# Optimization experiments

Hardware: AMD Instinct MI355X
Metric: run time of the kernel (lower is better)

## Reference

```python
import jax, jax.numpy as jnp
import numpy as np

B, C, H, W = 8, 512, 64, 32
SE_MID = C // 16
BN_EPS = 1e-5


def conv1x1(x, w, b):
    # x: [B,Cin,H,W], w: [Cout,Cin], b: [Cout]
    return jnp.einsum('bchw,oc->bohw', x, w) + b[None, :, None, None]


def setup_inputs() -> dict:
    key = jax.random.key(0)
    ks = jax.random.split(key, 17)
    s = 0.05
    return {
        'x': jax.random.normal(ks[0], (B, C, H, W), jnp.float32),
        'g_w': jax.random.normal(ks[1], (1, C), jnp.float32) * s,
        'g_b': jax.random.normal(ks[2], (1,), jnp.float32) * s,
        'theta_w': jax.random.normal(ks[3], (1, C), jnp.float32) * s,
        'theta_b': jax.random.normal(ks[4], (1,), jnp.float32) * s,
        'phi_w': jax.random.normal(ks[5], (1, C), jnp.float32) * s,
        'phi_b': jax.random.normal(ks[6], (1,), jnp.float32) * s,
        'W_w': jax.random.normal(ks[7], (C, 1), jnp.float32) * s,
        'W_b': jax.random.normal(ks[8], (C,), jnp.float32) * s,
        'bn_gamma': jax.random.normal(ks[9], (C,), jnp.float32) * s + 1.0,
        'bn_beta': jax.random.normal(ks[10], (C,), jnp.float32) * s,
        'bn_mean': jax.random.normal(ks[11], (C,), jnp.float32) * s,
        'bn_var': jax.random.uniform(ks[12], (C,), jnp.float32, 0.5, 1.5),
        'se1_w': jax.random.normal(ks[13], (SE_MID, C), jnp.float32) * s,
        'se1_b': jnp.zeros((SE_MID,), jnp.float32),
        'se2_w': jax.random.normal(ks[14], (C, SE_MID), jnp.float32) * s,
        'se2_b': jnp.zeros((C,), jnp.float32),
    }


def reference(x, g_w, g_b, theta_w, theta_b, phi_w, phi_b, W_w, W_b,
              bn_gamma, bn_beta, bn_mean, bn_var, se1_w, se1_b, se2_w, se2_b):
    b, c, h, w = x.shape
    N = h * w
    # SE channel gate from global average pool: [B,C,1,1]
    x_avg = jnp.mean(x, axis=(2, 3), keepdims=True)
    se_mid = jax.nn.relu(conv1x1(x_avg, se1_w, se1_b))
    W_cw = jax.nn.sigmoid(conv1x1(se_mid, se2_w, se2_b))  # [B,C,1,1]

    # inter_channels == 1: each projection is a length-N vector per sample
    g_x = conv1x1(x, g_w, g_b).reshape(b, N)          # [B,N]
    theta_x = conv1x1(x, theta_w, theta_b).reshape(b, N)  # [B,N]
    phi_x = conv1x1(x, phi_w, phi_b).reshape(b, N)        # [B,N]

    # f[b,i,j] = theta[b,i] * phi[b,j]; row softmax over j; y = f_div_C @ g
    f = theta_x[:, :, None] * phi_x[:, None, :]       # [B,N,N]
    f_div_C = jax.nn.softmax(f, axis=-1)
    y = jnp.einsum('bij,bj->bi', f_div_C, g_x)        # [B,N]
    y = y.reshape(b, 1, h, w)

    # W: 1x1 conv (1 -> C) + BatchNorm2d (inference form with running stats)
    W_y = conv1x1(y, W_w, W_b)                        # [B,C,H,W]
    inv = bn_gamma / jnp.sqrt(bn_var + BN_EPS)
    W_y = (W_y - bn_mean[None, :, None, None]) * inv[None, :, None, None] \
          + bn_beta[None, :, None, None]

    return W_cw * W_y + x
```

## Files before the change

kernel.cpp:

```cpp
#include <hip/hip_runtime.h>

#define BB 8
#define CC 512
#define NN 2048
#define SEM 32
#define BN_EPS 1e-5f

#define NCC 16
#define NCHUNK (CC / NCC)
#define PIX 1024

__global__ __launch_bounds__(256) void k1(const float* __restrict__ x,
    const float* __restrict__ gw, const float* __restrict__ tw, const float* __restrict__ pw,
    float* __restrict__ pp,
    float* __restrict__ avgp)
{
    int tid = threadIdx.x;
    int wave = tid >> 6, lane = tid & 63;
    int blk = blockIdx.x;
    int ic = blk & 1;
    int cc = (blk >> 1) & (NCHUNK - 1);
    int b  = blk >> 6;
    int c0 = cc * NCC;

    const float4* xp = reinterpret_cast<const float4*>(x)
                     + ((size_t)(b * CC + c0) * (NN / 4)) + ic * (PIX / 4);

    float4 ag = {0,0,0,0}, at_ = {0,0,0,0}, ap = {0,0,0,0};

    #pragma unroll 4
    for (int c = 0; c < NCC; ++c) {
        float4 v = xp[(size_t)c * (NN / 4) + tid];
        float wgc = gw[c0 + c], wtc = tw[c0 + c], wpc = pw[c0 + c];
        ag.x = fmaf(wgc, v.x, ag.x); ag.y = fmaf(wgc, v.y, ag.y);
        ag.z = fmaf(wgc, v.z, ag.z); ag.w = fmaf(wgc, v.w, ag.w);
        at_.x = fmaf(wtc, v.x, at_.x); at_.y = fmaf(wtc, v.y, at_.y);
        at_.z = fmaf(wtc, v.z, at_.z); at_.w = fmaf(wtc, v.w, at_.w);
        ap.x = fmaf(wpc, v.x, ap.x); ap.y = fmaf(wpc, v.y, ap.y);
        ap.z = fmaf(wpc, v.z, ap.z); ap.w = fmaf(wpc, v.w, ap.w);
        float s = (v.x + v.y) + (v.z + v.w);
        for (int o = 32; o > 0; o >>= 1) s += __shfl_down(s, o);
        if (lane == 0)
            avgp[(size_t)(b * CC + c0 + c) * 8 + ic * 4 + wave] = s;
    }

    size_t base = (((size_t)b * 2 + ic) * NCHUNK + cc) * PIX + tid * 4;
    const size_t karr = (size_t)BB * 2 * NCHUNK * PIX;
    *reinterpret_cast<float4*>(pp + 0 * karr + base) = ag;
    *reinterpret_cast<float4*>(pp + 1 * karr + base) = at_;
    *reinterpret_cast<float4*>(pp + 2 * karr + base) = ap;
}

__global__ __launch_bounds__(256) void k2(
    const float* __restrict__ pp, const float* __restrict__ avgp,
    const float* __restrict__ gb, const float* __restrict__ tb, const float* __restrict__ pb,
    const float* __restrict__ se1w, const float* __restrict__ se1b,
    const float* __restrict__ se2w, const float* __restrict__ se2b,
    const float* __restrict__ Ww, const float* __restrict__ Wb,
    const float* __restrict__ gamma, const float* __restrict__ beta,
    const float* __restrict__ mean, const float* __restrict__ var,
    float* __restrict__ gx, float* __restrict__ tx, float* __restrict__ px,
    float* __restrict__ Ac, float* __restrict__ Dc)
{
    int tid = threadIdx.x;
    if (blockIdx.x < 64) {
        int q  = blockIdx.x & 3;
        int ic = (blockIdx.x >> 2) & 1;
        int b  = blockIdx.x >> 3;
        int p  = q * 256 + tid;
        size_t base = (((size_t)b * 2 + ic) * NCHUNK) * PIX + p;
        const size_t karr = (size_t)BB * 2 * NCHUNK * PIX;
        float g = 0.f, t = 0.f, ph = 0.f;
        #pragma unroll 8
        for (int cc = 0; cc < NCHUNK; ++cc) {
            g  += pp[0 * karr + base + cc * PIX];
            t  += pp[1 * karr + base + cc * PIX];
            ph += pp[2 * karr + base + cc * PIX];
        }
        int o = b * NN + ic * PIX + p;
        gx[o] = g + gb[0];
        tx[o] = t + tb[0];
        px[o] = ph + pb[0];
        return;
    }

    int b = blockIdx.x - 64;
    __shared__ float sA[CC];
    __shared__ float sP[SEM][8];
    __shared__ float sM[SEM];
    for (int c = tid; c < CC; c += 256) {
        const float* ap = avgp + (size_t)(b * CC + c) * 8;
        float s = 0.f;
        #pragma unroll
        for (int k = 0; k < 8; ++k) s += ap[k];
        sA[c] = s * (1.0f / NN);
    }
    __syncthreads();
    {
        int m = tid >> 3, sub = tid & 7;
        const float* w1 = se1w + m * CC + sub * 64;
        const float* a1 = sA + sub * 64;
        float s = 0.f;
        #pragma unroll
        for (int k = 0; k < 64; ++k) s = fmaf(a1[k], w1[k], s);
        sP[m][sub] = s;
    }
    __syncthreads();
    if (tid < SEM) {
        float t = 0.f;
        #pragma unroll
        for (int k = 0; k < 8; ++k) t += sP[tid][k];
        sM[tid] = fmaxf(t + se1b[tid], 0.f);
    }
    __syncthreads();
    for (int c = tid; c < CC; c += 256) {
        float s2 = 0.f;
        #pragma unroll
        for (int m = 0; m < SEM; ++m) s2 = fmaf(sM[m], se2w[c * SEM + m], s2);
        s2 += se2b[c];
        float wcw = 1.f / (1.f + __expf(-s2));
        float inv = gamma[c] * rsqrtf(var[c] + BN_EPS);
        Ac[b * CC + c] = wcw * Ww[c] * inv;
        Dc[b * CC + c] = wcw * ((Wb[c] - mean[c]) * inv + beta[c]);
    }
}

__global__ __launch_bounds__(256) void k3(
    const float* __restrict__ gx, const float* __restrict__ tx,
    const float* __restrict__ px, float* __restrict__ y)
{
    __shared__ float2 pg[NN];
    int tid = threadIdx.x;
    int b  = blockIdx.x >> 7;
    int i0 = (blockIdx.x & 127) << 4;
    for (int j = tid; j < NN; j += 256)
        pg[j] = make_float2(px[b * NN + j], gx[b * NN + j]);
    __syncthreads();

    int wave = tid >> 6, lane = tid & 63;
    int r0 = i0 + wave * 4;
    float t0 = tx[b * NN + r0 + 0];
    float t1 = tx[b * NN + r0 + 1];
    float t2 = tx[b * NN + r0 + 2];
    float t3 = tx[b * NN + r0 + 3];
    float s0 = 0.f, g0 = 0.f, s1 = 0.f, g1 = 0.f;
    float s2 = 0.f, g2 = 0.f, s3 = 0.f, g3 = 0.f;
    #pragma unroll 4
    for (int j = lane; j < NN; j += 64) {
        float2 v = pg[j];
        float e0 = __expf(fminf(t0 * v.x, 80.f));
        float e1 = __expf(fminf(t1 * v.x, 80.f));
        float e2 = __expf(fminf(t2 * v.x, 80.f));
        float e3 = __expf(fminf(t3 * v.x, 80.f));
        s0 += e0; g0 = fmaf(e0, v.y, g0);
        s1 += e1; g1 = fmaf(e1, v.y, g1);
        s2 += e2; g2 = fmaf(e2, v.y, g2);
        s3 += e3; g3 = fmaf(e3, v.y, g3);
    }
    for (int o = 32; o > 0; o >>= 1) {
        s0 += __shfl_down(s0, o); g0 += __shfl_down(g0, o);
        s1 += __shfl_down(s1, o); g1 += __shfl_down(g1, o);
        s2 += __shfl_down(s2, o); g2 += __shfl_down(g2, o);
        s3 += __shfl_down(s3, o); g3 += __shfl_down(g3, o);
    }
    if (lane == 0) {
        y[b * NN + r0 + 0] = g0 / s0;
        y[b * NN + r0 + 1] = g1 / s1;
        y[b * NN + r0 + 2] = g2 / s2;
        y[b * NN + r0 + 3] = g3 / s3;
    }
}

__global__ __launch_bounds__(256) void k4(
    const float* __restrict__ x, const float* __restrict__ y,
    const float* __restrict__ Ac, const float* __restrict__ Dc,
    float* __restrict__ out)
{
    int bc = blockIdx.x;
    int b = bc >> 9;
    float a = Ac[bc], d = Dc[bc];
    const float4* x4 = reinterpret_cast<const float4*>(x) + (size_t)bc * (NN / 4);
    const float4* y4 = reinterpret_cast<const float4*>(y) + (size_t)b * (NN / 4);
    float4* o4 = reinterpret_cast<float4*>(out) + (size_t)bc * (NN / 4);
    int tid = threadIdx.x;
    #pragma unroll
    for (int k = 0; k < 2; ++k) {
        int idx = k * 256 + tid;
        float4 xv = x4[idx], yv = y4[idx], ov;
        ov.x = fmaf(a, yv.x, d) + xv.x;
        ov.y = fmaf(a, yv.y, d) + xv.y;
        ov.z = fmaf(a, yv.z, d) + xv.z;
        ov.w = fmaf(a, yv.w, d) + xv.w;
        o4[idx] = ov;
    }
}

extern "C" void kernel_launch(void* const* d_in, const int* in_sizes, int n_in,
                              void* d_out, int out_size, void* d_ws, size_t ws_size,
                              hipStream_t stream) {
    const float* x    = (const float*)d_in[0];
    const float* gw   = (const float*)d_in[1];
    const float* gb   = (const float*)d_in[2];
    const float* tw   = (const float*)d_in[3];
    const float* tb   = (const float*)d_in[4];
    const float* pw   = (const float*)d_in[5];
    const float* pb   = (const float*)d_in[6];
    const float* Ww   = (const float*)d_in[7];
    const float* Wb   = (const float*)d_in[8];
    const float* gam  = (const float*)d_in[9];
    const float* bet  = (const float*)d_in[10];
    const float* mu   = (const float*)d_in[11];
    const float* var  = (const float*)d_in[12];
    const float* se1w = (const float*)d_in[13];
    const float* se1b = (const float*)d_in[14];
    const float* se2w = (const float*)d_in[15];
    const float* se2b = (const float*)d_in[16];

    float* ws   = (float*)d_ws;
    float* pp   = ws; ws += 3 * BB * 2 * NCHUNK * PIX;
    float* avgp = ws; ws += BB * CC * 8;
    float* gx   = ws; ws += BB * NN;
    float* tx   = ws; ws += BB * NN;
    float* px   = ws; ws += BB * NN;
    float* y    = ws; ws += BB * NN;
    float* Ac   = ws; ws += BB * CC;
    float* Dc   = ws; ws += BB * CC;
    float* out  = (float*)d_out;

    k1<<<BB * NCHUNK * 2, 256, 0, stream>>>(x, gw, tw, pw, pp, avgp);
    k2<<<64 + BB, 256, 0, stream>>>(pp, avgp, gb, tb, pb, se1w, se1b, se2w, se2b,
                                    Ww, Wb, gam, bet, mu, var, gx, tx, px, Ac, Dc);
    k3<<<BB * 128, 256, 0, stream>>>(gx, tx, px, y);
    k4<<<BB * CC, 256, 0, stream>>>(x, y, Ac, Dc, out);
}
```

Before: 42.51 us.

## Batch k1 channel-sum shuffles, vectorize k2 reduction, move SE gate into softmax kernel

```diff
diff --git a/kernel.cpp b/kernel.cpp
--- a/kernel.cpp
+++ b/kernel.cpp
@@ -27,8 +27,9 @@
                      + ((size_t)(b * CC + c0) * (NN / 4)) + ic * (PIX / 4);
 
     float4 ag = {0,0,0,0}, at_ = {0,0,0,0}, ap = {0,0,0,0};
-
-    #pragma unroll 4
+    float s[NCC];
+
+    #pragma unroll
     for (int c = 0; c < NCC; ++c) {
         float4 v = xp[(size_t)c * (NN / 4) + tid];
         float wgc = gw[c0 + c], wtc = tw[c0 + c], wpc = pw[c0 + c];
@@ -38,10 +39,7 @@
         at_.z = fmaf(wtc, v.z, at_.z); at_.w = fmaf(wtc, v.w, at_.w);
         ap.x = fmaf(wpc, v.x, ap.x); ap.y = fmaf(wpc, v.y, ap.y);
         ap.z = fmaf(wpc, v.z, ap.z); ap.w = fmaf(wpc, v.w, ap.w);
-        float s = (v.x + v.y) + (v.z + v.w);
-        for (int o = 32; o > 0; o >>= 1) s += __shfl_down(s, o);
-        if (lane == 0)
-            avgp[(size_t)(b * CC + c0 + c) * 8 + ic * 4 + wave] = s;
+        s[c] = (v.x + v.y) + (v.z + v.w);
     }
 
     size_t base = (((size_t)b * 2 + ic) * NCHUNK + cc) * PIX + tid * 4;
@@ -49,88 +47,106 @@
     *reinterpret_cast<float4*>(pp + 0 * karr + base) = ag;
     *reinterpret_cast<float4*>(pp + 1 * karr + base) = at_;
     *reinterpret_cast<float4*>(pp + 2 * karr + base) = ap;
+
+    #pragma unroll
+    for (int o = 32; o > 0; o >>= 1) {
+        #pragma unroll
+        for (int c = 0; c < NCC; ++c)
+            s[c] += __shfl_down(s[c], o);
+    }
+    if (lane == 0) {
+        #pragma unroll
+        for (int c = 0; c < NCC; ++c)
+            avgp[(size_t)(b * CC + c0 + c) * 8 + ic * 4 + wave] = s[c];
+    }
 }
 
 __global__ __launch_bounds__(256) void k2(
-    const float* __restrict__ pp, const float* __restrict__ avgp,
+    const float* __restrict__ pp,
     const float* __restrict__ gb, const float* __restrict__ tb, const float* __restrict__ pb,
+    float* __restrict__ gx, float* __restrict__ tx, float* __restrict__ px)
+{
+    int tid = threadIdx.x;
+    int half = blockIdx.x & 1;
+    int ic   = (blockIdx.x >> 1) & 1;
+    int b    = blockIdx.x >> 2;
+    int p    = half * 512 + tid * 2;
+    size_t base = ((((size_t)b * 2 + ic) * NCHUNK) * PIX + p) / 2;
+    const size_t karr2 = (size_t)BB * 2 * NCHUNK * PIX / 2;
+    const float2* pp2 = reinterpret_cast<const float2*>(pp);
+    float2 g = {0,0}, t = {0,0}, ph = {0,0};
+    #pragma unroll 8
+    for (int cc = 0; cc < NCHUNK; ++cc) {
+        float2 a = pp2[0 * karr2 + base + cc * (PIX / 2)];
+        float2 c = pp2[1 * karr2 + base + cc * (PIX / 2)];
+        float2 d = pp2[2 * karr2 + base + cc * (PIX / 2)];
+        g.x += a.x;  g.y += a.y;
+        t.x += c.x;  t.y += c.y;
+        ph.x += d.x; ph.y += d.y;
+    }
+    int o = b * NN + ic * PIX + p;
+    float gbv = gb[0], tbv = tb[0], pbv = pb[0];
+    *reinterpret_cast<float2*>(gx + o) = make_float2(g.x + gbv, g.y + gbv);
+    *reinterpret_cast<float2*>(tx + o) = make_float2(t.x + tbv, t.y + tbv);
+    *reinterpret_cast<float2*>(px + o) = make_float2(ph.x + pbv, ph.y + pbv);
+}
+
+__global__ __launch_bounds__(256) void k3(
+    const float* __restrict__ gx, const float* __restrict__ tx,
+    const float* __restrict__ px, const float* __restrict__ avgp,
     const float* __restrict__ se1w, const float* __restrict__ se1b,
     const float* __restrict__ se2w, const float* __restrict__ se2b,
     const float* __restrict__ Ww, const float* __restrict__ Wb,
     const float* __restrict__ gamma, const float* __restrict__ beta,
     const float* __restrict__ mean, const float* __restrict__ var,
-    float* __restrict__ gx, float* __restrict__ tx, float* __restrict__ px,
-    float* __restrict__ Ac, float* __restrict__ Dc)
-{
-    int tid = threadIdx.x;
-    if (blockIdx.x < 64) {
-        int q  = blockIdx.x & 3;
-        int ic = (blockIdx.x >> 2) & 1;
-        int b  = blockIdx.x >> 3;
-        int p  = q * 256 + tid;
-        size_t base = (((size_t)b * 2 + ic) * NCHUNK) * PIX + p;
-        const size_t karr = (size_t)BB * 2 * NCHUNK * PIX;
-        float g = 0.f, t = 0.f, ph = 0.f;
-        #pragma unroll 8
-        for (int cc = 0; cc < NCHUNK; ++cc) {
-            g  += pp[0 * karr + base + cc * PIX];
-            t  += pp[1 * karr + base + cc * PIX];
-            ph += pp[2 * karr + base + cc * PIX];
-        }
-        int o = b * NN + ic * PIX + p;
-        gx[o] = g + gb[0];
-        tx[o] = t + tb[0];
-        px[o] = ph + pb[0];
+    float* __restrict__ y, float* __restrict__ Ac, float* __restrict__ Dc)
+{
+    int tid = threadIdx.x;
+
+    if (blockIdx.x >= 1024) {
+        int b = blockIdx.x - 1024;
+        __shared__ float sA[CC];
+        __shared__ float sP[SEM][8];
+        __shared__ float sM[SEM];
+        for (int c = tid; c < CC; c += 256) {
+            const float* apt = avgp + (size_t)(b * CC + c) * 8;
+            float s = 0.f;
+            #pragma unroll
+            for (int k = 0; k < 8; ++k) s += apt[k];
+            sA[c] = s * (1.0f / NN);
+        }
+        __syncthreads();
+        {
+            int m = tid >> 3, sub = tid & 7;
+            const float* w1 = se1w + m * CC + sub * 64;
+            const float* a1 = sA + sub * 64;
+            float s = 0.f;
+            #pragma unroll
+            for (int k = 0; k < 64; ++k) s = fmaf(a1[k], w1[k], s);
+            sP[m][sub] = s;
+        }
+        __syncthreads();
+        if (tid < SEM) {
+            float t = 0.f;
+            #pragma unroll
+            for (int k = 0; k < 8; ++k) t += sP[tid][k];
+            sM[tid] = fmaxf(t + se1b[tid], 0.f);
+        }
+        __syncthreads();
+        for (int c = tid; c < CC; c += 256) {
+            float s2 = 0.f;
+            #pragma unroll
+            for (int m = 0; m < SEM; ++m) s2 = fmaf(sM[m], se2w[c * SEM + m], s2);
+            s2 += se2b[c];
+            float wcw = 1.f / (1.f + __expf(-s2));
+            float inv = gamma[c] * rsqrtf(var[c] + BN_EPS);
+            Ac[b * CC + c] = wcw * Ww[c] * inv;
+            Dc[b * CC + c] = wcw * ((Wb[c] - mean[c]) * inv + beta[c]);
+        }
         return;
     }
 
-    int b = blockIdx.x - 64;
-    __shared__ float sA[CC];
-    __shared__ float sP[SEM][8];
-    __shared__ float sM[SEM];
-    for (int c = tid; c < CC; c += 256) {
-        const float* ap = avgp + (size_t)(b * CC + c) * 8;
-        float s = 0.f;
-        #pragma unroll
-        for (int k = 0; k < 8; ++k) s += ap[k];
-        sA[c] = s * (1.0f / NN);
-    }
-    __syncthreads();
-    {
-        int m = tid >> 3, sub = tid & 7;
-        const float* w1 = se1w + m * CC + sub * 64;
-        const float* a1 = sA + sub * 64;
-        float s = 0.f;
-        #pragma unroll
-        for (int k = 0; k < 64; ++k) s = fmaf(a1[k], w1[k], s);
-        sP[m][sub] = s;
-    }
-    __syncthreads();
-    if (tid < SEM) {
-        float t = 0.f;
-        #pragma unroll
-        for (int k = 0; k < 8; ++k) t += sP[tid][k];
-        sM[tid] = fmaxf(t + se1b[tid], 0.f);
-    }
-    __syncthreads();
-    for (int c = tid; c < CC; c += 256) {
-        float s2 = 0.f;
-        #pragma unroll
-        for (int m = 0; m < SEM; ++m) s2 = fmaf(sM[m], se2w[c * SEM + m], s2);
-        s2 += se2b[c];
-        float wcw = 1.f / (1.f + __expf(-s2));
-        float inv = gamma[c] * rsqrtf(var[c] + BN_EPS);
-        Ac[b * CC + c] = wcw * Ww[c] * inv;
-        Dc[b * CC + c] = wcw * ((Wb[c] - mean[c]) * inv + beta[c]);
-    }
-}
-
-__global__ __launch_bounds__(256) void k3(
-    const float* __restrict__ gx, const float* __restrict__ tx,
-    const float* __restrict__ px, float* __restrict__ y)
-{
     __shared__ float2 pg[NN];
-    int tid = threadIdx.x;
     int b  = blockIdx.x >> 7;
     int i0 = (blockIdx.x & 127) << 4;
     for (int j = tid; j < NN; j += 256)
@@ -228,8 +244,8 @@
     float* out  = (float*)d_out;
 
     k1<<<BB * NCHUNK * 2, 256, 0, stream>>>(x, gw, tw, pw, pp, avgp);
-    k2<<<64 + BB, 256, 0, stream>>>(pp, avgp, gb, tb, pb, se1w, se1b, se2w, se2b,
-                                    Ww, Wb, gam, bet, mu, var, gx, tx, px, Ac, Dc);
-    k3<<<BB * 128, 256, 0, stream>>>(gx, tx, px, y);
+    k2<<<BB * 2 * 2, 256, 0, stream>>>(pp, gb, tb, pb, gx, tx, px);
+    k3<<<1024 + BB, 256, 0, stream>>>(gx, tx, px, avgp, se1w, se1b, se2w, se2b,
+                                      Ww, Wb, gam, bet, mu, var, y, Ac, Dc);
     k4<<<BB * CC, 256, 0, stream>>>(x, y, Ac, Dc, out);
 }
```

Measured after the change: 39.19 us. -7.8%, faster.
